# Performance work log

Hardware: AMD Instinct MI355X
Metric: run time of the kernel (lower is better)

The kernel has to match this reference:

```python
import jax, jax.numpy as jnp
import numpy as np
import math

HEAD_SIZE = 64
WINDOW = 512  # sliding_window_size


def setup_inputs() -> dict:
    key = jax.random.key(0)
    k1, k2, k3, k4 = jax.random.split(key, 4)
    B, T, C = 4, 4096, 1024
    x = jax.random.normal(k1, (B, T, C), dtype=jnp.float32)
    # torch nn.Linear(C, head_size, bias=False) computes x @ W.T with W [hs, C];
    # we store the transposed [C, hs] layout so projection is x @ w.
    s = 1.0 / math.sqrt(C)
    w_key = jax.random.uniform(k2, (C, HEAD_SIZE), jnp.float32, -s, s)
    w_query = jax.random.uniform(k3, (C, HEAD_SIZE), jnp.float32, -s, s)
    w_value = jax.random.uniform(k4, (C, HEAD_SIZE), jnp.float32, -s, s)
    return {"x": x, "w_key": w_key, "w_query": w_query, "w_value": w_value}


def reference(x, w_key, w_query, w_value):
    # Non-cache path (use_cache=False): keys/values are the fresh projections,
    # q_start = k_start = 0, win_size = sliding_window_size.
    B, T, C = x.shape
    q = x @ w_query          # [B, T, hs]
    k = x @ w_key            # [B, T, hs]
    v = x @ w_value          # [B, T, hs]

    # attn_scores = q @ k^T  -> [B, T, T]
    scores = jnp.einsum('btd,bsd->bts', q, k)

    # Sliding-window causal mask: invalid where diff < 0 or diff >= window,
    # with diff = q_pos - k_pos.
    pos = jnp.arange(T)
    diff = pos[:, None] - pos[None, :]          # [T, T]
    mask_bool = (diff < 0) | (diff >= WINDOW)

    scale = math.sqrt(HEAD_SIZE)
    scores = jnp.where(mask_bool[None, :, :], -jnp.inf, scores)
    attn = jax.nn.softmax(scores / scale, axis=-1)  # dropout p=0.0 -> identity

    out = jnp.einsum('bts,bsd->btd', attn, v)   # [B, T, hs]
    return out
```

## Files before the change

### kernel.cpp

```cpp
#include <hip/hip_runtime.h>
#include <hip/hip_bf16.h>
#include <math.h>

#define BB 4
#define TT 4096
#define CC 1024
#define HS 64
#define WIN 512
#define NROW (BB*TT)

typedef float f32x4 __attribute__((ext_vector_type(4)));
typedef short bf16x8 __attribute__((ext_vector_type(8)));

#define MFMA16(a, b, c) __builtin_amdgcn_mfma_f32_16x16x32_bf16((a), (b), (c), 0, 0, 0)

#define GLOAD_LDS(gp, lp) __builtin_amdgcn_global_load_lds( \
    (const __attribute__((address_space(1))) void*)(gp), \
    (__attribute__((address_space(3))) void*)(lp), 16, 0, 0)

__device__ inline unsigned short f2b(float f) {
  union { __hip_bfloat16 h; unsigned short u; } v;
  v.h = __float2bfloat16(f);
  return v.u;
}

__global__ __launch_bounds__(256) void pack_w_kernel(
    const float* __restrict__ wq, const float* __restrict__ wk,
    const float* __restrict__ wv, unsigned short* __restrict__ wp)
{
  int t = blockIdx.x * 256 + threadIdx.x;
  int kg = t / 48;
  int nq = t % 48;
  int n0 = nq * 4;
  int m  = n0 >> 6;
  int c  = n0 & 63;
  const float* w = (m == 0) ? wq : (m == 1) ? wk : wv;
  float4 v = *(const float4*)&w[(size_t)kg * HS + c];
  int kt = kg >> 5;
  int hi = (kg >> 3) & 3;
  int j  = kg & 7;
  float vals[4] = {v.x, v.y, v.z, v.w};
  #pragma unroll
  for (int i = 0; i < 4; ++i) {
    int n  = n0 + i;
    int nb = n >> 4;
    int rl = n & 15;
    int lane = hi * 16 + rl;
    wp[((size_t)(kt * 12 + nb) * 64 + lane) * 8 + j] = f2b(vals[i]);
  }
}

__global__ __launch_bounds__(512) void proj_mfma_kernel(
    const float* __restrict__ x, const unsigned short* __restrict__ wp,
    unsigned short* __restrict__ q_ws, unsigned short* __restrict__ k_ws,
    unsigned short* __restrict__ vt_ws)
{
  __shared__ unsigned char xbuf[4][16384];
  __shared__ unsigned char wbuf[2][24576];

  const int tid = threadIdx.x;
  const int l   = tid & 63;
  const int wid = tid >> 6;
  const int cq  = wid & 3;
  const int rh  = wid >> 2;
  const int rl  = l & 15;
  const int hi  = l >> 4;
  const int r0  = blockIdx.x * 64;

  f32x4 acc[2][3];
  #pragma unroll
  for (int g = 0; g < 2; ++g)
    #pragma unroll
    for (int j = 0; j < 3; ++j) acc[g][j] = (f32x4){0.f, 0.f, 0.f, 0.f};

#define SX(KS, BUF) { \
    _Pragma("unroll") \
    for (int r = 0; r < 2; ++r) { \
      int s    = r * 512 + tid; \
      int row  = s >> 4; \
      int cpos = s & 15; \
      int cg   = cpos ^ ((row & 7) << 1); \
      GLOAD_LDS(x + (size_t)(r0 + row) * CC + (KS) * 64 + cg * 4, \
                &xbuf[BUF][s * 16]); \
    } }

#define LWR(KS, WR) { \
    _Pragma("unroll") \
    for (int i = 0; i < 3; ++i) \
      WR[i] = *(const bf16x8*)(wp + (size_t)(KS) * 12288 + (i * 512 + tid) * 8); }

#define WST(WR, BUF) { \
    _Pragma("unroll") \
    for (int i = 0; i < 3; ++i) \
      *(bf16x8*)&wbuf[BUF][(i * 512 + tid) * 16] = WR[i]; }

#define COMP(XB, WB) { \
    _Pragma("unroll") \
    for (int ktl = 0; ktl < 2; ++ktl) { \
      bf16x8 afr[2]; \
      _Pragma("unroll") \
      for (int g = 0; g < 2; ++g) { \
        int row = rh * 32 + g * 16 + rl; \
        int sw  = (row & 7) << 1; \
        int c0  = ktl * 8 + hi * 2; \
        const unsigned char* rb = &xbuf[XB][row * 256]; \
        f32x4 a0 = *(const f32x4*)(rb + ((c0 ^ sw) * 16)); \
        f32x4 a1 = *(const f32x4*)(rb + (((c0 + 1) ^ sw) * 16)); \
        bf16x8 af; \
        af[0] = (short)f2b(a0[0]); af[1] = (short)f2b(a0[1]); \
        af[2] = (short)f2b(a0[2]); af[3] = (short)f2b(a0[3]); \
        af[4] = (short)f2b(a1[0]); af[5] = (short)f2b(a1[1]); \
        af[6] = (short)f2b(a1[2]); af[7] = (short)f2b(a1[3]); \
        afr[g] = af; \
      } \
      _Pragma("unroll") \
      for (int j = 0; j < 3; ++j) { \
        bf16x8 wf = *(const bf16x8*)&wbuf[WB][((ktl * 12 + cq * 3 + j) * 64 + l) * 16]; \
        acc[0][j] = MFMA16(afr[0], wf, acc[0][j]); \
        acc[1][j] = MFMA16(afr[1], wf, acc[1][j]); \
      } \
    } }

#define PHASE_END { \
    asm volatile("s_waitcnt lgkmcnt(0)" ::: "memory"); \
    __builtin_amdgcn_sched_barrier(0); \
    __builtin_amdgcn_s_barrier(); }

  bf16x8 wrA[3], wrB[3];

  SX(0, 0) SX(1, 1) SX(2, 2)
  LWR(0, wrA)
  WST(wrA, 0)
  LWR(1, wrB)
  PHASE_END

  #pragma unroll 1
  for (int ks = 0; ks < 16; ks += 2) {
    if (ks + 3 <= 15) { SX(ks + 3, (ks + 3) & 3) }
    if (ks + 2 <= 15) { LWR(ks + 2, wrA) }
    if (ks + 1 <= 15) { WST(wrB, (ks + 1) & 1) }
    COMP(ks & 3, ks & 1)
    PHASE_END
    if (ks + 4 <= 15) { SX(ks + 4, (ks + 4) & 3) }
    if (ks + 3 <= 15) { LWR(ks + 3, wrB) }
    if (ks + 2 <= 15) { WST(wrA, (ks + 2) & 1) }
    COMP((ks + 1) & 3, (ks + 1) & 1)
    PHASE_END
  }
#undef SX
#undef LWR
#undef WST
#undef COMP
#undef PHASE_END

  #pragma unroll
  for (int g = 0; g < 2; ++g) {
    int rb = r0 + rh * 32 + g * 16;
    #pragma unroll
    for (int j = 0; j < 3; ++j) {
      int nb = cq * 3 + j;
      if (nb < 8) {
        unsigned short* dst = (nb < 4) ? q_ws : k_ws;
        int c = (nb & 3) * 16 + rl;
        #pragma unroll
        for (int r = 0; r < 4; ++r) {
          int row = rb + hi * 4 + r;
          dst[(size_t)row * HS + c] = f2b(acc[g][j][r]);
        }
      } else {
        int ch   = rb >> 6;
        int key0 = (rb & 63) + hi * 4;
        int d = (nb - 8) * 16 + rl;
        unsigned u0 = (unsigned)f2b(acc[g][j][0]) | ((unsigned)f2b(acc[g][j][1]) << 16);
        unsigned u1 = (unsigned)f2b(acc[g][j][2]) | ((unsigned)f2b(acc[g][j][3]) << 16);
        uint2 uu; uu.x = u0; uu.y = u1;
        *(uint2*)(vt_ws + (size_t)ch * 4096 + d * 64 + key0) = uu;
      }
    }
  }
}

__global__ __launch_bounds__(256) void attn_mfma_kernel(
    const unsigned short* __restrict__ q_ws, const unsigned short* __restrict__ k_ws,
    const unsigned short* __restrict__ vt_ws, float* __restrict__ out)
{
  __shared__ uint4 smem4[1600];
  unsigned char* smem = (unsigned char*)smem4;

  const int tid = threadIdx.x;
  const int l   = tid & 63;
  const int wid = tid >> 6;
  const int rl  = l & 15;
  const int hi  = l >> 4;
  const int b   = blockIdx.x >> 6;
  const int qt  = blockIdx.x & 63;
  const int t0  = qt * 64;
  const int t0w = t0 + wid * 16;

  const unsigned short* qrow = q_ws + (size_t)(b * TT + t0w + rl) * HS;
  bf16x8 qb0 = *(const bf16x8*)(qrow + hi * 8);
  bf16x8 qb1 = *(const bf16x8*)(qrow + 32 + hi * 8);

  f32x4 oacc[4];
  #pragma unroll
  for (int i = 0; i < 4; ++i) oacc[i] = (f32x4){0.f, 0.f, 0.f, 0.f};
  float m_run = -INFINITY, l_run = 0.f;

  int s_lo = t0 - WIN; if (s_lo < 0) s_lo = 0;
  unsigned char* pbase = smem + 16384 + wid * 2304 + rl * 144;

  for (int sc = s_lo; sc < t0 + 64; sc += 64) {
    __syncthreads();
    {
      const unsigned short* kg = k_ws + (size_t)(b * TT + sc) * HS;
      const unsigned short* vg = vt_ws + (size_t)((b * TT + sc) >> 6) * 4096;
      #pragma unroll
      for (int i = 0; i < 2; ++i) {
        int idx = tid + i * 256;
        int row = idx >> 3;
        int c16 = idx & 7;
        uint4 kv = *(const uint4*)(kg + row * 64 + c16 * 8);
        uint4 vv = *(const uint4*)(vg + row * 64 + c16 * 8);
        *(uint4*)(smem + row * 128 + ((c16 ^ (row & 7)) * 16)) = kv;
        *(uint4*)(smem + 8192 + row * 128 + ((c16 ^ (row & 7)) * 16)) = vv;
      }
    }
    __syncthreads();

    f32x4 sacc[4];
    #pragma unroll
    for (int i = 0; i < 4; ++i) sacc[i] = (f32x4){0.f, 0.f, 0.f, 0.f};
    #pragma unroll
    for (int kb = 0; kb < 4; ++kb) {
      int row = kb * 16 + rl;
      unsigned char* kr = smem + row * 128;
      bf16x8 k0 = *(const bf16x8*)(kr + (((hi) ^ (row & 7)) * 16));
      bf16x8 k1 = *(const bf16x8*)(kr + (((4 + hi) ^ (row & 7)) * 16));
      sacc[kb] = MFMA16(k0, qb0, sacc[kb]);
      sacc[kb] = MFMA16(k1, qb1, sacc[kb]);
    }

    const int tg = t0w + rl;
    float p[16];
    float tm = -INFINITY;
    bool full = (sc + 63 <= t0w) && (sc >= t0w - 496);
    #pragma unroll
    for (int kb = 0; kb < 4; ++kb)
      #pragma unroll
      for (int r = 0; r < 4; ++r) {
        float v = sacc[kb][r] * 0.125f;
        if (!full) {
          int key = sc + kb * 16 + hi * 4 + r;
          int diff = tg - key;
          v = (diff >= 0 && diff < WIN) ? v : -INFINITY;
        }
        p[kb * 4 + r] = v;
        tm = fmaxf(tm, v);
      }
    tm = fmaxf(tm, __shfl_xor(tm, 16));
    tm = fmaxf(tm, __shfl_xor(tm, 32));
    float m_new = fmaxf(m_run, tm);
    float fac  = (m_new == -INFINITY) ? 1.f : __expf(m_run - m_new);
    float msub = (m_new == -INFINITY) ? 0.f : m_new;
    float lsum = 0.f;
    #pragma unroll
    for (int i = 0; i < 16; ++i) { p[i] = __expf(p[i] - msub); lsum += p[i]; }
    lsum += __shfl_xor(lsum, 16);
    lsum += __shfl_xor(lsum, 32);
    l_run = l_run * fac + lsum;
    m_run = m_new;

    #pragma unroll
    for (int kb = 0; kb < 4; ++kb) {
      unsigned u0 = (unsigned)f2b(p[kb * 4 + 0]) | ((unsigned)f2b(p[kb * 4 + 1]) << 16);
      unsigned u1 = (unsigned)f2b(p[kb * 4 + 2]) | ((unsigned)f2b(p[kb * 4 + 3]) << 16);
      uint2 uu; uu.x = u0; uu.y = u1;
      *(uint2*)(pbase + kb * 32 + hi * 8) = uu;
    }

    #pragma unroll
    for (int r = 0; r < 4; ++r) {
      float fr = __shfl(fac, (l & 48) | (hi * 4 + r));
      oacc[0][r] *= fr; oacc[1][r] *= fr; oacc[2][r] *= fr; oacc[3][r] *= fr;
    }

    bf16x8 pa0 = *(const bf16x8*)(pbase + hi * 16);
    bf16x8 pa1 = *(const bf16x8*)(pbase + 64 + hi * 16);
    #pragma unroll
    for (int f = 0; f < 4; ++f) {
      int d = f * 16 + rl;
      unsigned char* vr = smem + 8192 + d * 128;
      bf16x8 v0 = *(const bf16x8*)(vr + (((hi) ^ (d & 7)) * 16));
      bf16x8 v1 = *(const bf16x8*)(vr + (((4 + hi) ^ (d & 7)) * 16));
      oacc[f] = MFMA16(pa0, v0, oacc[f]);
      oacc[f] = MFMA16(pa1, v1, oacc[f]);
    }
  }

  float inv = 1.f / l_run;
  #pragma unroll
  for (int r = 0; r < 4; ++r) {
    float ir = __shfl(inv, (l & 48) | (hi * 4 + r));
    int row = b * TT + t0w + hi * 4 + r;
    #pragma unroll
    for (int f = 0; f < 4; ++f)
      out[(size_t)row * HS + f * 16 + rl] = oacc[f][r] * ir;
  }
}

extern "C" void kernel_launch(void* const* d_in, const int* in_sizes, int n_in,
                              void* d_out, int out_size, void* d_ws, size_t ws_size,
                              hipStream_t stream) {
  const float* x  = (const float*)d_in[0];
  const float* wk = (const float*)d_in[1];
  const float* wq = (const float*)d_in[2];
  const float* wv = (const float*)d_in[3];
  float* out = (float*)d_out;

  unsigned short* wp    = (unsigned short*)d_ws;
  unsigned short* q_ws  = wp + 196608;
  unsigned short* k_ws  = q_ws + (size_t)NROW * HS;
  unsigned short* vt_ws = k_ws + (size_t)NROW * HS;

  pack_w_kernel<<<192, 256, 0, stream>>>(wq, wk, wv, wp);
  proj_mfma_kernel<<<NROW / 64, 512, 0, stream>>>(x, wp, q_ws, k_ws, vt_ws);
  attn_mfma_kernel<<<BB * (TT / 64), 256, 0, stream>>>(q_ws, k_ws, vt_ws, out);
}
```

Measured before the change: 49.29 us.

## Convert x to bf16 once at staging and double-buffer 128-wide K steps

The projection kernel now loads x tiles into registers, converts them to bf16 once and stores packed bf16 into swizzled LDS. Previously raw fp32 went to LDS via global_load_lds and every wave converted it again at fragment-load time. Weights are now streamed straight to LDS with global_load_lds instead of through registers, and the K loop becomes 8 double-buffered steps of 128 columns using a 128KB shared buffer. The goal is to remove redundant conversions and halve LDS traffic for x. The cost is very high LDS use, which limits occupancy to one block per CU, a shallower prefetch pipeline, and register staging of x.

```diff
diff --git a/kernel.cpp b/kernel.cpp
--- a/kernel.cpp
+++ b/kernel.cpp
@@ -55,8 +55,11 @@
     unsigned short* __restrict__ q_ws, unsigned short* __restrict__ k_ws,
     unsigned short* __restrict__ vt_ws)
 {
-  __shared__ unsigned char xbuf[4][16384];
-  __shared__ unsigned char wbuf[2][24576];
+  __shared__ unsigned char lds[131072];
+  unsigned char* const xb0 = lds;
+  unsigned char* const xb1 = lds + 16384;
+  unsigned char* const wb0 = lds + 32768;
+  unsigned char* const wb1 = lds + 81920;
 
   const int tid = threadIdx.x;
   const int l   = tid & 63;
@@ -73,85 +76,76 @@
     #pragma unroll
     for (int j = 0; j < 3; ++j) acc[g][j] = (f32x4){0.f, 0.f, 0.f, 0.f};
 
-#define SX(KS, BUF) { \
+  f32x4 xr[2][2];
+
+#define SXL(KS) { \
     _Pragma("unroll") \
-    for (int r = 0; r < 2; ++r) { \
-      int s    = r * 512 + tid; \
-      int row  = s >> 4; \
-      int cpos = s & 15; \
-      int cg   = cpos ^ ((row & 7) << 1); \
-      GLOAD_LDS(x + (size_t)(r0 + row) * CC + (KS) * 64 + cg * 4, \
-                &xbuf[BUF][s * 16]); \
+    for (int it = 0; it < 2; ++it) { \
+      int u = it * 512 + tid; \
+      const float* gp = x + (size_t)(r0 + (u >> 4)) * CC + (KS) * 128 + (u & 15) * 8; \
+      xr[it][0] = *(const f32x4*)gp; \
+      xr[it][1] = *(const f32x4*)(gp + 4); \
     } }
 
-#define LWR(KS, WR) { \
+#define XPACK(XB) { \
     _Pragma("unroll") \
-    for (int i = 0; i < 3; ++i) \
-      WR[i] = *(const bf16x8*)(wp + (size_t)(KS) * 12288 + (i * 512 + tid) * 8); }
-
-#define WST(WR, BUF) { \
+    for (int it = 0; it < 2; ++it) { \
+      int u = it * 512 + tid; \
+      int row = u >> 4, seg = u & 15; \
+      uint4 pk; \
+      pk.x = (unsigned)f2b(xr[it][0][0]) | ((unsigned)f2b(xr[it][0][1]) << 16); \
+      pk.y = (unsigned)f2b(xr[it][0][2]) | ((unsigned)f2b(xr[it][0][3]) << 16); \
+      pk.z = (unsigned)f2b(xr[it][1][0]) | ((unsigned)f2b(xr[it][1][1]) << 16); \
+      pk.w = (unsigned)f2b(xr[it][1][2]) | ((unsigned)f2b(xr[it][1][3]) << 16); \
+      *(uint4*)((XB) + row * 256 + (((seg ^ (row & 7))) << 4)) = pk; \
+    } }
+
+#define SW(KS, WB) { \
+    const unsigned short* wsrc = wp + (size_t)(KS) * 24576; \
     _Pragma("unroll") \
-    for (int i = 0; i < 3; ++i) \
-      *(bf16x8*)&wbuf[BUF][(i * 512 + tid) * 16] = WR[i]; }
+    for (int i = 0; i < 6; ++i) { \
+      int s = i * 512 + tid; \
+      GLOAD_LDS(wsrc + s * 8, (WB) + s * 16); \
+    } }
 
 #define COMP(XB, WB) { \
     _Pragma("unroll") \
-    for (int ktl = 0; ktl < 2; ++ktl) { \
+    for (int kt = 0; kt < 4; ++kt) { \
       bf16x8 afr[2]; \
       _Pragma("unroll") \
       for (int g = 0; g < 2; ++g) { \
         int row = rh * 32 + g * 16 + rl; \
-        int sw  = (row & 7) << 1; \
-        int c0  = ktl * 8 + hi * 2; \
-        const unsigned char* rb = &xbuf[XB][row * 256]; \
-        f32x4 a0 = *(const f32x4*)(rb + ((c0 ^ sw) * 16)); \
-        f32x4 a1 = *(const f32x4*)(rb + (((c0 + 1) ^ sw) * 16)); \
-        bf16x8 af; \
-        af[0] = (short)f2b(a0[0]); af[1] = (short)f2b(a0[1]); \
-        af[2] = (short)f2b(a0[2]); af[3] = (short)f2b(a0[3]); \
-        af[4] = (short)f2b(a1[0]); af[5] = (short)f2b(a1[1]); \
-        af[6] = (short)f2b(a1[2]); af[7] = (short)f2b(a1[3]); \
-        afr[g] = af; \
+        int seg = kt * 4 + hi; \
+        afr[g] = *(const bf16x8*)((XB) + row * 256 + ((seg ^ (row & 7)) << 4)); \
       } \
       _Pragma("unroll") \
       for (int j = 0; j < 3; ++j) { \
-        bf16x8 wf = *(const bf16x8*)&wbuf[WB][((ktl * 12 + cq * 3 + j) * 64 + l) * 16]; \
+        bf16x8 wf = *(const bf16x8*)((WB) + ((kt * 12 + cq * 3 + j) * 64 + l) * 16); \
         acc[0][j] = MFMA16(afr[0], wf, acc[0][j]); \
         acc[1][j] = MFMA16(afr[1], wf, acc[1][j]); \
       } \
     } }
 
-#define PHASE_END { \
-    asm volatile("s_waitcnt lgkmcnt(0)" ::: "memory"); \
-    __builtin_amdgcn_sched_barrier(0); \
-    __builtin_amdgcn_s_barrier(); }
-
-  bf16x8 wrA[3], wrB[3];
-
-  SX(0, 0) SX(1, 1) SX(2, 2)
-  LWR(0, wrA)
-  WST(wrA, 0)
-  LWR(1, wrB)
-  PHASE_END
-
-  #pragma unroll 1
-  for (int ks = 0; ks < 16; ks += 2) {
-    if (ks + 3 <= 15) { SX(ks + 3, (ks + 3) & 3) }
-    if (ks + 2 <= 15) { LWR(ks + 2, wrA) }
-    if (ks + 1 <= 15) { WST(wrB, (ks + 1) & 1) }
-    COMP(ks & 3, ks & 1)
-    PHASE_END
-    if (ks + 4 <= 15) { SX(ks + 4, (ks + 4) & 3) }
-    if (ks + 3 <= 15) { LWR(ks + 3, wrB) }
-    if (ks + 2 <= 15) { WST(wrA, (ks + 2) & 1) }
-    COMP((ks + 1) & 3, (ks + 1) & 1)
-    PHASE_END
-  }
-#undef SX
-#undef LWR
-#undef WST
+  SXL(0)
+  SW(0, wb0)
+  XPACK(xb0)
+  __syncthreads();
+
+  #pragma unroll
+  for (int ks = 0; ks < 8; ++ks) {
+    unsigned char* const xc = (ks & 1) ? xb1 : xb0;
+    unsigned char* const wc = (ks & 1) ? wb1 : wb0;
+    unsigned char* const xn = (ks & 1) ? xb0 : xb1;
+    unsigned char* const wn = (ks & 1) ? wb0 : wb1;
+    if (ks < 7) { SXL(ks + 1) SW(ks + 1, wn) }
+    COMP(xc, wc)
+    if (ks < 7) { XPACK(xn) }
+    __syncthreads();
+  }
+#undef SXL
+#undef XPACK
+#undef SW
 #undef COMP
-#undef PHASE_END
 
   #pragma unroll
   for (int g = 0; g < 2; ++g) {
```

Result: faster. 44.56 us (-9.6%).
